# Kernel optimization log

Hardware: AMD Instinct MI355X
Metric: run time of the kernel (lower is better)

The kernel has to match this reference:

```python
import jax, jax.numpy as jnp
import numpy as np

N_NODES = 100000
N_EDGES = 1600000
D_IN, D_HID, D_LAT = 128, 128, 64


def setup_inputs() -> dict:
    key = jax.random.key(0)
    ks = jax.random.split(key, 8)
    x = jax.random.normal(ks[0], (N_NODES, D_IN), dtype=jnp.float32)
    edge_index = jax.random.randint(ks[1], (2, N_EDGES), 0, N_NODES, dtype=jnp.int64)
    s1 = 1.0 / np.sqrt(D_IN)
    s2 = 1.0 / np.sqrt(D_HID)
    return {
        "x": x,
        "edge_index": edge_index,
        "W1_l": jax.random.normal(ks[2], (D_IN, D_HID), dtype=jnp.float32) * s1,
        "W1_r": jax.random.normal(ks[3], (D_IN, D_HID), dtype=jnp.float32) * s1,
        "b1": jnp.zeros((D_HID,), dtype=jnp.float32),
        "W2_l": jax.random.normal(ks[4], (D_HID, D_LAT), dtype=jnp.float32) * s2,
        "W2_r": jax.random.normal(ks[5], (D_HID, D_LAT), dtype=jnp.float32) * s2,
        "b2": jnp.zeros((D_LAT,), dtype=jnp.float32),
    }


def _sage_conv_mean(x, src, dst, W_l, W_r, b):
    """PyG SAGEConv with mean aggregation: lin_l(mean_j x_j) + lin_r(x_i)."""
    n = x.shape[0]
    # scatter-mean of source features into destination nodes
    agg = jax.ops.segment_sum(x[src], dst, num_segments=n)           # [N, d]
    deg = jax.ops.segment_sum(jnp.ones_like(dst, dtype=x.dtype), dst, num_segments=n)
    mean = agg / jnp.maximum(deg, 1.0)[:, None]
    return mean @ W_l + b + x @ W_r


def reference(x, edge_index, W1_l, W1_r, b1, W2_l, W2_r, b2):
    src, dst = edge_index[0], edge_index[1]
    h = jax.nn.relu(_sage_conv_mean(x, src, dst, W1_l, W1_r, b1))
    # Dropout(p=0.2) is identity in eval mode
    z = jax.nn.relu(_sage_conv_mean(h, src, dst, W2_l, W2_r, b2))
    return z
```

## Files before the change

kernel.cpp:

```cpp
#include <hip/hip_runtime.h>

#define N_NODES 100000
#define N_EDGES 1600000
#define D_IN 128
#define D_HID 128
#define D_LAT 64

#define BSHIFT 8
#define NB 392
#define CAP 4608
#define EPB 4096
#define PART_BLOCKS ((N_EDGES + EPB - 1) / EPB)

typedef unsigned short ushort_t;
typedef unsigned int uint_t;
typedef unsigned char uchar_t;
using bf16x8 = __attribute__((ext_vector_type(8))) short;
using f32x4  = __attribute__((ext_vector_type(4))) float;
using f32x2  = __attribute__((ext_vector_type(2))) float;

__device__ inline ushort_t f2bf(float f) {
    uint_t u = __float_as_uint(f);
    return (ushort_t)((u + 0x7fffu + ((u >> 16) & 1u)) >> 16);
}
__device__ inline uint_t pack2bf(float a, float b) {
    return (uint_t)f2bf(a) | ((uint_t)f2bf(b) << 16);
}
__device__ inline float bf2f(ushort_t u) {
    return __uint_as_float(((uint_t)u) << 16);
}

#if __has_builtin(__builtin_amdgcn_cvt_pk_f32_fp8) && __has_builtin(__builtin_amdgcn_cvt_pk_fp8_f32)
#define HW_FP8 1
template<bool HI>
__device__ inline f32x2 fp8pk2f(uint_t v) {
    return __builtin_amdgcn_cvt_pk_f32_fp8(v, HI);
}
__device__ inline uint_t f2fp8pk4(float a, float b, float c, float d) {
    uint_t w = __builtin_amdgcn_cvt_pk_fp8_f32(a, b, 0, false);
    w = __builtin_amdgcn_cvt_pk_fp8_f32(c, d, w, true);
    return w;
}
__device__ inline uchar_t f2fp8_byte(float f) {
    return (uchar_t)(__builtin_amdgcn_cvt_pk_fp8_f32(f, f, 0, false) & 0xff);
}
#else
__device__ inline float fp8b2f(uint_t b) {
    uint_t em = b & 0x7f;
    if (em == 0) return 0.f;
    uint_t bits = ((em << 20) + (120u << 23)) | ((b & 0x80u) << 24);
    return __uint_as_float(bits);
}
template<bool HI>
__device__ inline f32x2 fp8pk2f(uint_t v) {
    uint_t w = HI ? (v >> 16) : v;
    f32x2 r; r.x = fp8b2f(w & 0xff); r.y = fp8b2f((w >> 8) & 0xff);
    return r;
}
__device__ inline uint_t f2fp8_1(float f) {
    uint_t u = __float_as_uint(f);
    uint_t s = (u >> 31) << 7;
    uint_t au = u & 0x7fffffff;
    if (au >= 0x43e00000u) return s | 0x7e;
    if (au < 0x3c000000u) return s;
    uint_t r = au + 0x0007ffffu + ((au >> 20) & 1u);
    return s | (((r >> 20) - (120u << 3)) & 0x7f);
}
__device__ inline uint_t f2fp8pk4(float a, float b, float c, float d) {
    return f2fp8_1(a) | (f2fp8_1(b) << 8) | (f2fp8_1(c) << 16) | (f2fp8_1(d) << 24);
}
__device__ inline uchar_t f2fp8_byte(float f) { return (uchar_t)f2fp8_1(f); }
#endif

__device__ inline void accf8x4(float* a, uint_t w, int base) {
    f32x2 p0 = fp8pk2f<false>(w);
    f32x2 p1 = fp8pk2f<true>(w);
    a[base + 0] += p0.x; a[base + 1] += p0.y;
    a[base + 2] += p1.x; a[base + 3] += p1.y;
}
__device__ inline void accf8x16(float* a, uint4 u) {
    accf8x4(a, u.x, 0); accf8x4(a, u.y, 4); accf8x4(a, u.z, 8); accf8x4(a, u.w, 12);
}

__device__ inline void pack_w256(const float* Wl, const float* Wr, ushort_t* pack,
                                 int N, int tid) {
    int lane = tid & 63;
    int t = tid >> 6;
    int kt = t & 7;
    int nt = t >> 3;
    int n = nt * 16 + (lane & 15);
    int kbase = kt * 32 + (lane >> 4) * 8;
    ushort_t v[8];
    #pragma unroll
    for (int j = 0; j < 8; ++j) {
        int k = kbase + j;
        float w = (k < 128) ? Wl[k * N + n] : Wr[(k - 128) * N + n];
        v[j] = f2bf(w);
    }
    *(uint4*)(pack + (long)tid * 8) = *(uint4*)v;
}
__device__ inline void pack_w128(const float* W, ushort_t* pack, int N, int tid) {
    int lane = tid & 63;
    int t = tid >> 6;
    int kt = t & 3;
    int nt = t >> 2;
    int n = nt * 16 + (lane & 15);
    int kbase = kt * 32 + (lane >> 4) * 8;
    ushort_t v[8];
    #pragma unroll
    for (int j = 0; j < 8; ++j) v[j] = f2bf(W[(kbase + j) * N + n]);
    *(uint4*)(pack + (long)tid * 8) = *(uint4*)v;
}

__global__ __launch_bounds__(256) void prep_kernel(
        const float* __restrict__ W1_l, const float* __restrict__ W1_r,
        ushort_t* __restrict__ pack1,
        const float* __restrict__ W2_l, ushort_t* __restrict__ pack2l,
        const float* __restrict__ W2_r, ushort_t* __restrict__ pack2r,
        int* __restrict__ gCur) {
    int b = blockIdx.x;
    if (b < 16) {
        pack_w256(W1_l, W1_r, pack1, 128, b * 256 + threadIdx.x);
    } else if (b < 20) {
        pack_w128(W2_l, pack2l, 64, (b - 16) * 256 + threadIdx.x);
    } else if (b < 24) {
        pack_w128(W2_r, pack2r, 64, (b - 20) * 256 + threadIdx.x);
    } else {
        int t = (b - 24) * 256 + threadIdx.x;
        if (t < NB) gCur[t] = t * CAP;
    }
}

__global__ __launch_bounds__(256) void bucket_scatter_kernel(const int* __restrict__ src,
                                                             const int* __restrict__ dst,
                                                             int* __restrict__ gCur,
                                                             int* __restrict__ bedges) {
    __shared__ int h[NB];
    __shared__ int start[NB];
    for (int j = threadIdx.x; j < NB; j += 256) h[j] = 0;
    __syncthreads();
    long base = (long)blockIdx.x * EPB + threadIdx.x * 16;
    int dc[16], sc[16];
    int cnt = 0;
    if (base + 16 <= N_EDGES) {
        #pragma unroll
        for (int j = 0; j < 4; ++j) {
            int4 d4 = *(const int4*)(dst + base + j * 4);
            int4 s4 = *(const int4*)(src + base + j * 4);
            dc[j * 4 + 0] = d4.x; dc[j * 4 + 1] = d4.y; dc[j * 4 + 2] = d4.z; dc[j * 4 + 3] = d4.w;
            sc[j * 4 + 0] = s4.x; sc[j * 4 + 1] = s4.y; sc[j * 4 + 2] = s4.z; sc[j * 4 + 3] = s4.w;
        }
        cnt = 16;
    } else if (base < N_EDGES) {
        cnt = (int)(N_EDGES - base);
        for (int j = 0; j < cnt; ++j) { dc[j] = dst[base + j]; sc[j] = src[base + j]; }
    }
    for (int j = 0; j < cnt; ++j) atomicAdd(&h[dc[j] >> BSHIFT], 1);
    __syncthreads();
    for (int j = threadIdx.x; j < NB; j += 256)
        start[j] = h[j] ? atomicAdd(&gCur[j], h[j]) : 0;
    __syncthreads();
    for (int j = 0; j < cnt; ++j) {
        int b = dc[j] >> BSHIFT;
        int p = atomicAdd(&start[b], 1);
        if (p < (b + 1) * CAP)
            bedges[p] = ((dc[j] & 255) << 24) | sc[j];
    }
}

__global__ __launch_bounds__(256) void bucket_sort_kernel(const int* __restrict__ gCur,
                                                          const int* __restrict__ bedges,
                                                          int* __restrict__ csr,
                                                          int2* __restrict__ off2) {
    __shared__ int sdata[256];
    __shared__ int cur[256];
    int b = blockIdx.x, t = threadIdx.x;
    int r0 = b * CAP;
    int n = gCur[b] - r0;
    if (n > CAP) n = CAP;
    cur[t] = 0;
    __syncthreads();
    for (int k = t * 4; k < n; k += 1024) {
        int4 v4 = *(const int4*)(bedges + r0 + k);
        int m = n - k;
        atomicAdd(&cur[(unsigned)v4.x >> 24], 1);
        if (m > 1) atomicAdd(&cur[(unsigned)v4.y >> 24], 1);
        if (m > 2) atomicAdd(&cur[(unsigned)v4.z >> 24], 1);
        if (m > 3) atomicAdd(&cur[(unsigned)v4.w >> 24], 1);
    }
    __syncthreads();
    int c = cur[t];
    sdata[t] = c;
    __syncthreads();
    for (int d = 1; d < 256; d <<= 1) {
        int u = (t >= d) ? sdata[t - d] : 0;
        __syncthreads();
        sdata[t] += u;
        __syncthreads();
    }
    int ex = (t == 0) ? 0 : sdata[t - 1];
    off2[(b << BSHIFT) + t] = make_int2(r0 + ex, c);
    cur[t] = ex;
    __syncthreads();
    for (int k = t * 4; k < n; k += 1024) {
        int4 v4 = *(const int4*)(bedges + r0 + k);
        int m = n - k;
        {
            int p = atomicAdd(&cur[(unsigned)v4.x >> 24], 1);
            csr[r0 + p] = v4.x & 0xFFFFFF;
        }
        if (m > 1) {
            int p = atomicAdd(&cur[(unsigned)v4.y >> 24], 1);
            csr[r0 + p] = v4.y & 0xFFFFFF;
        }
        if (m > 2) {
            int p = atomicAdd(&cur[(unsigned)v4.z >> 24], 1);
            csr[r0 + p] = v4.z & 0xFFFFFF;
        }
        if (m > 3) {
            int p = atomicAdd(&cur[(unsigned)v4.w >> 24], 1);
            csr[r0 + p] = v4.w & 0xFFFFFF;
        }
    }
}

__global__ void cvt_both_kernel(const float* __restrict__ in, ushort_t* __restrict__ outb,
                                uchar_t* __restrict__ out8, long n) {
    long i = ((long)blockIdx.x * blockDim.x + threadIdx.x) * 16;
    if (i >= n) return;
    float4 a = *(const float4*)(in + i);
    float4 b = *(const float4*)(in + i + 4);
    float4 c = *(const float4*)(in + i + 8);
    float4 d = *(const float4*)(in + i + 12);
    uint4 ob0, ob1;
    ob0.x = pack2bf(a.x, a.y); ob0.y = pack2bf(a.z, a.w);
    ob0.z = pack2bf(b.x, b.y); ob0.w = pack2bf(b.z, b.w);
    ob1.x = pack2bf(c.x, c.y); ob1.y = pack2bf(c.z, c.w);
    ob1.z = pack2bf(d.x, d.y); ob1.w = pack2bf(d.z, d.w);
    *(uint4*)(outb + i) = ob0;
    *(uint4*)(outb + i + 8) = ob1;
    uint4 o8;
    o8.x = f2fp8pk4(a.x, a.y, a.z, a.w);
    o8.y = f2fp8pk4(b.x, b.y, b.z, b.w);
    o8.z = f2fp8pk4(c.x, c.y, c.z, c.w);
    o8.w = f2fp8pk4(d.x, d.y, d.z, d.w);
    *(uint4*)(out8 + i) = o8;
}

__global__ __launch_bounds__(256) void gather_mean_fp8_kernel(
        const int2* __restrict__ off2, const int* __restrict__ csr_src,
        const uchar_t* __restrict__ x8, ushort_t* __restrict__ mean_out) {
    int lane  = threadIdx.x & 7;
    int local = threadIdx.x >> 3;
    long i = (long)blockIdx.x * 32 + local;
    if (i >= N_NODES) return;
    int2 bd = off2[i];
    int beg = bd.x, n = bd.y;
    const uchar_t* base = x8 + lane * 16;
    float acc[16];
    #pragma unroll
    for (int j = 0; j < 16; ++j) acc[j] = 0.f;
    int k = 0;
    for (; k + 4 <= n; k += 4) {
        int s0 = csr_src[beg + k];
        int s1 = csr_src[beg + k + 1];
        int s2 = csr_src[beg + k + 2];
        int s3 = csr_src[beg + k + 3];
        uint4 u0 = *(const uint4*)(base + (long)s0 * 128);
        uint4 u1 = *(const uint4*)(base + (long)s1 * 128);
        uint4 u2 = *(const uint4*)(base + (long)s2 * 128);
        uint4 u3 = *(const uint4*)(base + (long)s3 * 128);
        accf8x16(acc, u0); accf8x16(acc, u1); accf8x16(acc, u2); accf8x16(acc, u3);
    }
    for (; k < n; ++k) {
        int s0 = csr_src[beg + k];
        uint4 u0 = *(const uint4*)(base + (long)s0 * 128);
        accf8x16(acc, u0);
    }
    float inv = (n > 0) ? 1.f / (float)n : 0.f;
    uint4 o0, o1;
    o0.x = pack2bf(acc[0] * inv,  acc[1] * inv);
    o0.y = pack2bf(acc[2] * inv,  acc[3] * inv);
    o0.z = pack2bf(acc[4] * inv,  acc[5] * inv);
    o0.w = pack2bf(acc[6] * inv,  acc[7] * inv);
    o1.x = pack2bf(acc[8] * inv,  acc[9] * inv);
    o1.y = pack2bf(acc[10] * inv, acc[11] * inv);
    o1.z = pack2bf(acc[12] * inv, acc[13] * inv);
    o1.w = pack2bf(acc[14] * inv, acc[15] * inv);
    ushort_t* mp = mean_out + i * 128 + lane * 16;
    *(uint4*)mp = o0;
    *(uint4*)(mp + 8) = o1;
}

__global__ __launch_bounds__(256) void gather_mean64_fp8_kernel(
        const int2* __restrict__ off2, const int* __restrict__ csr_src,
        const uchar_t* __restrict__ g8, ushort_t* __restrict__ mean_out) {
    int lane  = threadIdx.x & 3;
    int local = threadIdx.x >> 2;
    long i = (long)blockIdx.x * 64 + local;
    if (i >= N_NODES) return;
    int2 bd = off2[i];
    int beg = bd.x, n = bd.y;
    const uchar_t* base = g8 + lane * 16;
    float acc[16];
    #pragma unroll
    for (int j = 0; j < 16; ++j) acc[j] = 0.f;
    int k = 0;
    for (; k + 4 <= n; k += 4) {
        int s0 = csr_src[beg + k];
        int s1 = csr_src[beg + k + 1];
        int s2 = csr_src[beg + k + 2];
        int s3 = csr_src[beg + k + 3];
        uint4 u0 = *(const uint4*)(base + (long)s0 * 64);
        uint4 u1 = *(const uint4*)(base + (long)s1 * 64);
        uint4 u2 = *(const uint4*)(base + (long)s2 * 64);
        uint4 u3 = *(const uint4*)(base + (long)s3 * 64);
        accf8x16(acc, u0); accf8x16(acc, u1); accf8x16(acc, u2); accf8x16(acc, u3);
    }
    for (; k < n; ++k) {
        int s0 = csr_src[beg + k];
        uint4 u0 = *(const uint4*)(base + (long)s0 * 64);
        accf8x16(acc, u0);
    }
    float inv = (n > 0) ? 1.f / (float)n : 0.f;
    uint4 o0, o1;
    o0.x = pack2bf(acc[0] * inv,  acc[1] * inv);
    o0.y = pack2bf(acc[2] * inv,  acc[3] * inv);
    o0.z = pack2bf(acc[4] * inv,  acc[5] * inv);
    o0.w = pack2bf(acc[6] * inv,  acc[7] * inv);
    o1.x = pack2bf(acc[8] * inv,  acc[9] * inv);
    o1.y = pack2bf(acc[10] * inv, acc[11] * inv);
    o1.z = pack2bf(acc[12] * inv, acc[13] * inv);
    o1.w = pack2bf(acc[14] * inv, acc[15] * inv);
    ushort_t* mp = mean_out + i * 64 + lane * 16;
    *(uint4*)mp = o0;
    *(uint4*)(mp + 8) = o1;
}

template<int NOUT, bool OUT_BF16>
__global__ __launch_bounds__(256) void mfma_mlp_kernel(
        const ushort_t* __restrict__ Am, const ushort_t* __restrict__ Ax,
        const ushort_t* __restrict__ pack, const float* __restrict__ bias,
        void* __restrict__ outv) {
    constexpr int NT = NOUT / 16;
    int lane = threadIdx.x & 63;
    int wave = threadIdx.x >> 6;
    long m0 = (long)blockIdx.x * 64 + wave * 16;
    int r = lane & 15;
    int quad = lane >> 4;
    long arow = m0 + r;
    if (arow > N_NODES - 1) arow = N_NODES - 1;

    bf16x8 areg[8];
    #pragma unroll
    for (int kt = 0; kt < 8; ++kt) {
        const ushort_t* s = (kt < 4) ? Am : Ax;
        int k = (kt & 3) * 32 + quad * 8;
        areg[kt] = *(const bf16x8*)(s + arow * 128 + k);
    }

    f32x4 acc[NT];
    #pragma unroll
    for (int nt = 0; nt < NT; ++nt) acc[nt] = (f32x4){0.f, 0.f, 0.f, 0.f};

    #pragma unroll
    for (int nt = 0; nt < NT; ++nt) {
        #pragma unroll
        for (int kt = 0; kt < 8; ++kt) {
            bf16x8 bfrag = *(const bf16x8*)(pack + ((long)(nt * 8 + kt) * 64 + lane) * 8);
            acc[nt] = __builtin_amdgcn_mfma_f32_16x16x32_bf16(areg[kt], bfrag, acc[nt], 0, 0, 0);
        }
    }

    #pragma unroll
    for (int nt = 0; nt < NT; ++nt) {
        int col = nt * 16 + r;
        float bj = bias[col];
        #pragma unroll
        for (int q = 0; q < 4; ++q) {
            long orow = m0 + quad * 4 + q;
            if (orow < N_NODES) {
                float v = fmaxf(acc[nt][q] + bj, 0.f);
                if (OUT_BF16) ((ushort_t*)outv)[orow * NOUT + col] = f2bf(v);
                else          ((float*)outv)[orow * NOUT + col] = v;
            }
        }
    }
}

template<int NOUT, int OUTMODE, bool PRELOAD, bool HASBIAS, bool RELU>
__global__ __launch_bounds__(256) void mfma_gemm_k128_kernel(
        const ushort_t* __restrict__ A, const ushort_t* __restrict__ pack,
        const float* __restrict__ bias, const ushort_t* __restrict__ Cpre,
        void* __restrict__ outv) {
    constexpr int NT = NOUT / 16;
    int lane = threadIdx.x & 63;
    int wave = threadIdx.x >> 6;
    long m0 = (long)blockIdx.x * 64 + wave * 16;
    int r = lane & 15;
    int quad = lane >> 4;
    long arow = m0 + r;
    if (arow > N_NODES - 1) arow = N_NODES - 1;

    bf16x8 areg[4];
    #pragma unroll
    for (int kt = 0; kt < 4; ++kt)
        areg[kt] = *(const bf16x8*)(A + arow * 128 + kt * 32 + quad * 8);

    f32x4 acc[NT];
    #pragma unroll
    for (int nt = 0; nt < NT; ++nt) {
        if (PRELOAD) {
            int col = nt * 16 + r;
            #pragma unroll
            for (int q = 0; q < 4; ++q) {
                long row = m0 + quad * 4 + q;
                if (row > N_NODES - 1) row = N_NODES - 1;
                acc[nt][q] = bf2f(Cpre[row * NOUT + col]);
            }
        } else {
            acc[nt] = (f32x4){0.f, 0.f, 0.f, 0.f};
        }
    }

    #pragma unroll
    for (int nt = 0; nt < NT; ++nt) {
        #pragma unroll
        for (int kt = 0; kt < 4; ++kt) {
            bf16x8 bfrag = *(const bf16x8*)(pack + ((long)(nt * 4 + kt) * 64 + lane) * 8);
            acc[nt] = __builtin_amdgcn_mfma_f32_16x16x32_bf16(areg[kt], bfrag, acc[nt], 0, 0, 0);
        }
    }

    #pragma unroll
    for (int nt = 0; nt < NT; ++nt) {
        int col = nt * 16 + r;
        float bj = HASBIAS ? bias[col] : 0.f;
        #pragma unroll
        for (int q = 0; q < 4; ++q) {
            long orow = m0 + quad * 4 + q;
            if (orow < N_NODES) {
                float v = acc[nt][q] + bj;
                if (RELU) v = fmaxf(v, 0.f);
                if (OUTMODE == 2)      ((uchar_t*)outv)[orow * NOUT + col] = f2fp8_byte(v);
                else if (OUTMODE == 1) ((ushort_t*)outv)[orow * NOUT + col] = f2bf(v);
                else                   ((float*)outv)[orow * NOUT + col] = v;
            }
        }
    }
}

extern "C" void kernel_launch(void* const* d_in, const int* in_sizes, int n_in,
                              void* d_out, int out_size, void* d_ws, size_t ws_size,
                              hipStream_t stream) {
    const float* x    = (const float*)d_in[0];
    const int*   ei   = (const int*)d_in[1];
    const float* W1_l = (const float*)d_in[2];
    const float* W1_r = (const float*)d_in[3];
    const float* b1   = (const float*)d_in[4];
    const float* W2_l = (const float*)d_in[5];
    const float* W2_r = (const float*)d_in[6];
    const float* b2   = (const float*)d_in[7];
    float* out = (float*)d_out;

    const int* src = ei;
    const int* dst = ei + N_EDGES;

    int*  gCur   = (int*)d_ws;
    int2* off2   = (int2*)(gCur + 512);
    int*  bedges = (int*)(off2 + 100608);
    int*  csr    = bedges + NB * CAP;
    ushort_t* xb    = (ushort_t*)(csr + NB * CAP);
    ushort_t* mean1 = xb + (long)N_NODES * 128;
    uchar_t*  g8    = (uchar_t*)mean1;
    ushort_t* meang = mean1 + (long)N_NODES * 64;
    ushort_t* hb    = mean1 + (long)N_NODES * 128;
    uchar_t*  x8    = (uchar_t*)hb;
    ushort_t* pack1  = hb + (long)N_NODES * 128;
    ushort_t* pack2l = pack1 + 256 * 128;
    ushort_t* pack2r = pack2l + 128 * 64;

    prep_kernel<<<26, 256, 0, stream>>>(W1_l, W1_r, pack1, W2_l, pack2l, W2_r, pack2r, gCur);

    bucket_scatter_kernel<<<PART_BLOCKS, 256, 0, stream>>>(src, dst, gCur, bedges);
    bucket_sort_kernel<<<NB, 256, 0, stream>>>(gCur, bedges, csr, off2);

    cvt_both_kernel<<<((long)N_NODES * 128 / 16 + 255) / 256, 256, 0, stream>>>(
        x, xb, x8, (long)N_NODES * 128);

    gather_mean_fp8_kernel<<<(N_NODES + 31) / 32, 256, 0, stream>>>(off2, csr, x8, mean1);
    mfma_mlp_kernel<128, true><<<(N_NODES + 63) / 64, 256, 0, stream>>>(mean1, xb, pack1, b1, hb);

    mfma_gemm_k128_kernel<64, 2, false, false, false><<<(N_NODES + 63) / 64, 256, 0, stream>>>(
        hb, pack2l, nullptr, nullptr, g8);
    gather_mean64_fp8_kernel<<<(N_NODES + 63) / 64, 256, 0, stream>>>(off2, csr, g8, meang);
    mfma_gemm_k128_kernel<64, 0, true, true, true><<<(N_NODES + 63) / 64, 256, 0, stream>>>(
        hb, pack2r, b2, meang, out);
}
```

Baseline: 262.6 us.

## Fuse conversion into prep, layer-1 MLP with W2_l GEMM, and gather with final GEMM

Folds the x-to-bf16/fp8 conversion into the weight-prep launch. The layer-1 MLP kernel now stages its h tile in shared memory and immediately applies W2_l to produce the fp8 g tensor, so hb is not re-read for that GEMM. The second-layer gather-mean is merged with the final W2_r GEMM through a shared-memory mean tile, which removes the meang round trip through global memory and cuts two launches. In exchange the fused kernels use more shared memory and registers, which may lower occupancy, and the final kernel couples an irregular gather with MFMA work.

New measurement: 246.1 us (median of 2 runs). 1.07x faster.

```diff
diff --git a/kernel.cpp b/kernel.cpp
--- a/kernel.cpp
+++ b/kernel.cpp
@@ -11,6 +11,7 @@
 #define CAP 4608
 #define EPB 4096
 #define PART_BLOCKS ((N_EDGES + EPB - 1) / EPB)
+#define CVT_BLOCKS (((long)N_NODES * 128 / 16 + 255) / 256)
 
 typedef unsigned short ushort_t;
 typedef unsigned int uint_t;
@@ -117,7 +118,9 @@
         ushort_t* __restrict__ pack1,
         const float* __restrict__ W2_l, ushort_t* __restrict__ pack2l,
         const float* __restrict__ W2_r, ushort_t* __restrict__ pack2r,
-        int* __restrict__ gCur) {
+        int* __restrict__ gCur,
+        const float* __restrict__ x, ushort_t* __restrict__ xb,
+        uchar_t* __restrict__ x8) {
     int b = blockIdx.x;
     if (b < 16) {
         pack_w256(W1_l, W1_r, pack1, 128, b * 256 + threadIdx.x);
@@ -125,9 +128,29 @@
         pack_w128(W2_l, pack2l, 64, (b - 16) * 256 + threadIdx.x);
     } else if (b < 24) {
         pack_w128(W2_r, pack2r, 64, (b - 20) * 256 + threadIdx.x);
-    } else {
+    } else if (b < 26) {
         int t = (b - 24) * 256 + threadIdx.x;
         if (t < NB) gCur[t] = t * CAP;
+    } else {
+        long i = ((long)(b - 26) * 256 + threadIdx.x) * 16;
+        if (i >= (long)N_NODES * 128) return;
+        float4 a = *(const float4*)(x + i);
+        float4 bb = *(const float4*)(x + i + 4);
+        float4 c = *(const float4*)(x + i + 8);
+        float4 d = *(const float4*)(x + i + 12);
+        uint4 ob0, ob1;
+        ob0.x = pack2bf(a.x, a.y);  ob0.y = pack2bf(a.z, a.w);
+        ob0.z = pack2bf(bb.x, bb.y); ob0.w = pack2bf(bb.z, bb.w);
+        ob1.x = pack2bf(c.x, c.y);  ob1.y = pack2bf(c.z, c.w);
+        ob1.z = pack2bf(d.x, d.y);  ob1.w = pack2bf(d.z, d.w);
+        *(uint4*)(xb + i) = ob0;
+        *(uint4*)(xb + i + 8) = ob1;
+        uint4 o8;
+        o8.x = f2fp8pk4(a.x, a.y, a.z, a.w);
+        o8.y = f2fp8pk4(bb.x, bb.y, bb.z, bb.w);
+        o8.z = f2fp8pk4(c.x, c.y, c.z, c.w);
+        o8.w = f2fp8pk4(d.x, d.y, d.z, d.w);
+        *(uint4*)(x8 + i) = o8;
     }
 }
 
@@ -222,29 +245,6 @@
             csr[r0 + p] = v4.w & 0xFFFFFF;
         }
     }
-}
-
-__global__ void cvt_both_kernel(const float* __restrict__ in, ushort_t* __restrict__ outb,
-                                uchar_t* __restrict__ out8, long n) {
-    long i = ((long)blockIdx.x * blockDim.x + threadIdx.x) * 16;
-    if (i >= n) return;
-    float4 a = *(const float4*)(in + i);
-    float4 b = *(const float4*)(in + i + 4);
-    float4 c = *(const float4*)(in + i + 8);
-    float4 d = *(const float4*)(in + i + 12);
-    uint4 ob0, ob1;
-    ob0.x = pack2bf(a.x, a.y); ob0.y = pack2bf(a.z, a.w);
-    ob0.z = pack2bf(b.x, b.y); ob0.w = pack2bf(b.z, b.w);
-    ob1.x = pack2bf(c.x, c.y); ob1.y = pack2bf(c.z, c.w);
-    ob1.z = pack2bf(d.x, d.y); ob1.w = pack2bf(d.z, d.w);
-    *(uint4*)(outb + i) = ob0;
-    *(uint4*)(outb + i + 8) = ob1;
-    uint4 o8;
-    o8.x = f2fp8pk4(a.x, a.y, a.z, a.w);
-    o8.y = f2fp8pk4(b.x, b.y, b.z, b.w);
-    o8.z = f2fp8pk4(c.x, c.y, c.z, c.w);
-    o8.w = f2fp8pk4(d.x, d.y, d.z, d.w);
-    *(uint4*)(out8 + i) = o8;
 }
 
 __global__ __launch_bounds__(256) void gather_mean_fp8_kernel(
@@ -292,57 +292,13 @@
     *(uint4*)(mp + 8) = o1;
 }
 
-__global__ __launch_bounds__(256) void gather_mean64_fp8_kernel(
-        const int2* __restrict__ off2, const int* __restrict__ csr_src,
-        const uchar_t* __restrict__ g8, ushort_t* __restrict__ mean_out) {
-    int lane  = threadIdx.x & 3;
-    int local = threadIdx.x >> 2;
-    long i = (long)blockIdx.x * 64 + local;
-    if (i >= N_NODES) return;
-    int2 bd = off2[i];
-    int beg = bd.x, n = bd.y;
-    const uchar_t* base = g8 + lane * 16;
-    float acc[16];
-    #pragma unroll
-    for (int j = 0; j < 16; ++j) acc[j] = 0.f;
-    int k = 0;
-    for (; k + 4 <= n; k += 4) {
-        int s0 = csr_src[beg + k];
-        int s1 = csr_src[beg + k + 1];
-        int s2 = csr_src[beg + k + 2];
-        int s3 = csr_src[beg + k + 3];
-        uint4 u0 = *(const uint4*)(base + (long)s0 * 64);
-        uint4 u1 = *(const uint4*)(base + (long)s1 * 64);
-        uint4 u2 = *(const uint4*)(base + (long)s2 * 64);
-        uint4 u3 = *(const uint4*)(base + (long)s3 * 64);
-        accf8x16(acc, u0); accf8x16(acc, u1); accf8x16(acc, u2); accf8x16(acc, u3);
-    }
-    for (; k < n; ++k) {
-        int s0 = csr_src[beg + k];
-        uint4 u0 = *(const uint4*)(base + (long)s0 * 64);
-        accf8x16(acc, u0);
-    }
-    float inv = (n > 0) ? 1.f / (float)n : 0.f;
-    uint4 o0, o1;
-    o0.x = pack2bf(acc[0] * inv,  acc[1] * inv);
-    o0.y = pack2bf(acc[2] * inv,  acc[3] * inv);
-    o0.z = pack2bf(acc[4] * inv,  acc[5] * inv);
-    o0.w = pack2bf(acc[6] * inv,  acc[7] * inv);
-    o1.x = pack2bf(acc[8] * inv,  acc[9] * inv);
-    o1.y = pack2bf(acc[10] * inv, acc[11] * inv);
-    o1.z = pack2bf(acc[12] * inv, acc[13] * inv);
-    o1.w = pack2bf(acc[14] * inv, acc[15] * inv);
-    ushort_t* mp = mean_out + i * 64 + lane * 16;
-    *(uint4*)mp = o0;
-    *(uint4*)(mp + 8) = o1;
-}
-
-template<int NOUT, bool OUT_BF16>
-__global__ __launch_bounds__(256) void mfma_mlp_kernel(
+#define HSTRIDE 132
+__global__ __launch_bounds__(256) void mfma_mlp_fused_kernel(
         const ushort_t* __restrict__ Am, const ushort_t* __restrict__ Ax,
-        const ushort_t* __restrict__ pack, const float* __restrict__ bias,
-        void* __restrict__ outv) {
-    constexpr int NT = NOUT / 16;
+        const ushort_t* __restrict__ pack1, const float* __restrict__ bias,
+        const ushort_t* __restrict__ pack2l,
+        ushort_t* __restrict__ hb, uchar_t* __restrict__ g8) {
+    __shared__ ushort_t htile[4][16 * HSTRIDE];
     int lane = threadIdx.x & 63;
     int wave = threadIdx.x >> 6;
     long m0 = (long)blockIdx.x * 64 + wave * 16;
@@ -359,93 +315,148 @@
         areg[kt] = *(const bf16x8*)(s + arow * 128 + k);
     }
 
-    f32x4 acc[NT];
-    #pragma unroll
-    for (int nt = 0; nt < NT; ++nt) acc[nt] = (f32x4){0.f, 0.f, 0.f, 0.f};
-
-    #pragma unroll
-    for (int nt = 0; nt < NT; ++nt) {
+    f32x4 acc[8];
+    #pragma unroll
+    for (int nt = 0; nt < 8; ++nt) acc[nt] = (f32x4){0.f, 0.f, 0.f, 0.f};
+    #pragma unroll
+    for (int nt = 0; nt < 8; ++nt) {
         #pragma unroll
         for (int kt = 0; kt < 8; ++kt) {
-            bf16x8 bfrag = *(const bf16x8*)(pack + ((long)(nt * 8 + kt) * 64 + lane) * 8);
+            bf16x8 bfrag = *(const bf16x8*)(pack1 + ((long)(nt * 8 + kt) * 64 + lane) * 8);
             acc[nt] = __builtin_amdgcn_mfma_f32_16x16x32_bf16(areg[kt], bfrag, acc[nt], 0, 0, 0);
         }
     }
 
     #pragma unroll
-    for (int nt = 0; nt < NT; ++nt) {
+    for (int nt = 0; nt < 8; ++nt) {
         int col = nt * 16 + r;
         float bj = bias[col];
         #pragma unroll
         for (int q = 0; q < 4; ++q) {
             long orow = m0 + quad * 4 + q;
-            if (orow < N_NODES) {
-                float v = fmaxf(acc[nt][q] + bj, 0.f);
-                if (OUT_BF16) ((ushort_t*)outv)[orow * NOUT + col] = f2bf(v);
-                else          ((float*)outv)[orow * NOUT + col] = v;
-            }
-        }
-    }
-}
-
-template<int NOUT, int OUTMODE, bool PRELOAD, bool HASBIAS, bool RELU>
-__global__ __launch_bounds__(256) void mfma_gemm_k128_kernel(
-        const ushort_t* __restrict__ A, const ushort_t* __restrict__ pack,
-        const float* __restrict__ bias, const ushort_t* __restrict__ Cpre,
-        void* __restrict__ outv) {
-    constexpr int NT = NOUT / 16;
+            float v = fmaxf(acc[nt][q] + bj, 0.f);
+            ushort_t hv = f2bf(v);
+            if (orow < N_NODES) hb[orow * 128 + col] = hv;
+            htile[wave][(quad * 4 + q) * HSTRIDE + col] = hv;
+        }
+    }
+    bf16x8 areg2[4];
+    #pragma unroll
+    for (int kt = 0; kt < 4; ++kt)
+        areg2[kt] = *(const bf16x8*)(&htile[wave][r * HSTRIDE + kt * 32 + quad * 8]);
+    f32x4 gacc[4];
+    #pragma unroll
+    for (int nt = 0; nt < 4; ++nt) gacc[nt] = (f32x4){0.f, 0.f, 0.f, 0.f};
+    #pragma unroll
+    for (int nt = 0; nt < 4; ++nt) {
+        #pragma unroll
+        for (int kt = 0; kt < 4; ++kt) {
+            bf16x8 bfrag = *(const bf16x8*)(pack2l + ((long)(nt * 4 + kt) * 64 + lane) * 8);
+            gacc[nt] = __builtin_amdgcn_mfma_f32_16x16x32_bf16(areg2[kt], bfrag, gacc[nt], 0, 0, 0);
+        }
+    }
+    #pragma unroll
+    for (int nt = 0; nt < 4; ++nt) {
+        int col = nt * 16 + r;
+        #pragma unroll
+        for (int q = 0; q < 4; ++q) {
+            long orow = m0 + quad * 4 + q;
+            if (orow < N_NODES) g8[orow * 64 + col] = f2fp8_byte(gacc[nt][q]);
+        }
+    }
+}
+
+#define MSTRIDE 68
+__global__ __launch_bounds__(256) void mfma_final_kernel(
+        const int2* __restrict__ off2, const int* __restrict__ csr_src,
+        const uchar_t* __restrict__ g8,
+        const ushort_t* __restrict__ hb, const ushort_t* __restrict__ pack2r,
+        const float* __restrict__ b2, float* __restrict__ out) {
+    __shared__ ushort_t mtile[64 * MSTRIDE];
+    long m0 = (long)blockIdx.x * 64;
+    {
+        int lane  = threadIdx.x & 3;
+        int local = threadIdx.x >> 2;
+        long i = m0 + local;
+        if (i > N_NODES - 1) i = N_NODES - 1;
+        int2 bd = off2[i];
+        int beg = bd.x, n = bd.y;
+        const uchar_t* base = g8 + lane * 16;
+        float acc[16];
+        #pragma unroll
+        for (int j = 0; j < 16; ++j) acc[j] = 0.f;
+        int k = 0;
+        for (; k + 4 <= n; k += 4) {
+            int s0 = csr_src[beg + k];
+            int s1 = csr_src[beg + k + 1];
+            int s2 = csr_src[beg + k + 2];
+            int s3 = csr_src[beg + k + 3];
+            uint4 u0 = *(const uint4*)(base + (long)s0 * 64);
+            uint4 u1 = *(const uint4*)(base + (long)s1 * 64);
+            uint4 u2 = *(const uint4*)(base + (long)s2 * 64);
+            uint4 u3 = *(const uint4*)(base + (long)s3 * 64);
+            accf8x16(acc, u0); accf8x16(acc, u1); accf8x16(acc, u2); accf8x16(acc, u3);
+        }
+        for (; k < n; ++k) {
+            int s0 = csr_src[beg + k];
+            uint4 u0 = *(const uint4*)(base + (long)s0 * 64);
+            accf8x16(acc, u0);
+        }
+        float inv = (n > 0) ? 1.f / (float)n : 0.f;
+        uint4 o0, o1;
+        o0.x = pack2bf(acc[0] * inv,  acc[1] * inv);
+        o0.y = pack2bf(acc[2] * inv,  acc[3] * inv);
+        o0.z = pack2bf(acc[4] * inv,  acc[5] * inv);
+        o0.w = pack2bf(acc[6] * inv,  acc[7] * inv);
+        o1.x = pack2bf(acc[8] * inv,  acc[9] * inv);
+        o1.y = pack2bf(acc[10] * inv, acc[11] * inv);
+        o1.z = pack2bf(acc[12] * inv, acc[13] * inv);
+        o1.w = pack2bf(acc[14] * inv, acc[15] * inv);
+        ushort_t* mp = mtile + local * MSTRIDE + lane * 16;
+        *(uint4*)mp = o0;
+        *(uint4*)(mp + 8) = o1;
+    }
+    __syncthreads();
     int lane = threadIdx.x & 63;
     int wave = threadIdx.x >> 6;
-    long m0 = (long)blockIdx.x * 64 + wave * 16;
+    long mw = m0 + wave * 16;
     int r = lane & 15;
     int quad = lane >> 4;
-    long arow = m0 + r;
+    long arow = mw + r;
     if (arow > N_NODES - 1) arow = N_NODES - 1;
 
     bf16x8 areg[4];
     #pragma unroll
     for (int kt = 0; kt < 4; ++kt)
-        areg[kt] = *(const bf16x8*)(A + arow * 128 + kt * 32 + quad * 8);
-
-    f32x4 acc[NT];
-    #pragma unroll
-    for (int nt = 0; nt < NT; ++nt) {
-        if (PRELOAD) {
-            int col = nt * 16 + r;
-            #pragma unroll
-            for (int q = 0; q < 4; ++q) {
-                long row = m0 + quad * 4 + q;
-                if (row > N_NODES - 1) row = N_NODES - 1;
-                acc[nt][q] = bf2f(Cpre[row * NOUT + col]);
-            }
-        } else {
-            acc[nt] = (f32x4){0.f, 0.f, 0.f, 0.f};
-        }
-    }
-
-    #pragma unroll
-    for (int nt = 0; nt < NT; ++nt) {
+        areg[kt] = *(const bf16x8*)(hb + arow * 128 + kt * 32 + quad * 8);
+
+    f32x4 acc[4];
+    #pragma unroll
+    for (int nt = 0; nt < 4; ++nt) {
+        int col = nt * 16 + r;
+        #pragma unroll
+        for (int q = 0; q < 4; ++q) {
+            int rowl = wave * 16 + quad * 4 + q;
+            acc[nt][q] = bf2f(mtile[rowl * MSTRIDE + col]);
+        }
+    }
+    #pragma unroll
+    for (int nt = 0; nt < 4; ++nt) {
         #pragma unroll
         for (int kt = 0; kt < 4; ++kt) {
-            bf16x8 bfrag = *(const bf16x8*)(pack + ((long)(nt * 4 + kt) * 64 + lane) * 8);
+            bf16x8 bfrag = *(const bf16x8*)(pack2r + ((long)(nt * 4 + kt) * 64 + lane) * 8);
             acc[nt] = __builtin_amdgcn_mfma_f32_16x16x32_bf16(areg[kt], bfrag, acc[nt], 0, 0, 0);
         }
     }
-
-    #pragma unroll
-    for (int nt = 0; nt < NT; ++nt) {
+    #pragma unroll
+    for (int nt = 0; nt < 4; ++nt) {
         int col = nt * 16 + r;
-        float bj = HASBIAS ? bias[col] : 0.f;
+        float bj = b2[col];
         #pragma unroll
         for (int q = 0; q < 4; ++q) {
-            long orow = m0 + quad * 4 + q;
-            if (orow < N_NODES) {
-                float v = acc[nt][q] + bj;
-                if (RELU) v = fmaxf(v, 0.f);
-                if (OUTMODE == 2)      ((uchar_t*)outv)[orow * NOUT + col] = f2fp8_byte(v);
-                else if (OUTMODE == 1) ((ushort_t*)outv)[orow * NOUT + col] = f2bf(v);
-                else                   ((float*)outv)[orow * NOUT + col] = v;
-            }
+            long orow = mw + quad * 4 + q;
+            if (orow < N_NODES)
+                out[orow * 64 + col] = fmaxf(acc[nt][q] + bj, 0.f);
         }
     }
 }
@@ -472,28 +483,23 @@
     int*  csr    = bedges + NB * CAP;
     ushort_t* xb    = (ushort_t*)(csr + NB * CAP);
     ushort_t* mean1 = xb + (long)N_NODES * 128;
-    uchar_t*  g8    = (uchar_t*)mean1;
-    ushort_t* meang = mean1 + (long)N_NODES * 64;
     ushort_t* hb    = mean1 + (long)N_NODES * 128;
     uchar_t*  x8    = (uchar_t*)hb;
     ushort_t* pack1  = hb + (long)N_NODES * 128;
     ushort_t* pack2l = pack1 + 256 * 128;
     ushort_t* pack2r = pack2l + 128 * 64;
-
-    prep_kernel<<<26, 256, 0, stream>>>(W1_l, W1_r, pack1, W2_l, pack2l, W2_r, pack2r, gCur);
+    uchar_t*  g8     = (uchar_t*)(pack2r + 128 * 64);
+
+    prep_kernel<<<26 + CVT_BLOCKS, 256, 0, stream>>>(
+        W1_l, W1_r, pack1, W2_l, pack2l, W2_r, pack2r, gCur, x, xb, x8);
 
     bucket_scatter_kernel<<<PART_BLOCKS, 256, 0, stream>>>(src, dst, gCur, bedges);
     bucket_sort_kernel<<<NB, 256, 0, stream>>>(gCur, bedges, csr, off2);
 
-    cvt_both_kernel<<<((long)N_NODES * 128 / 16 + 255) / 256, 256, 0, stream>>>(
-        x, xb, x8, (long)N_NODES * 128);
-
     gather_mean_fp8_kernel<<<(N_NODES + 31) / 32, 256, 0, stream>>>(off2, csr, x8, mean1);
-    mfma_mlp_kernel<128, true><<<(N_NODES + 63) / 64, 256, 0, stream>>>(mean1, xb, pack1, b1, hb);
-
-    mfma_gemm_k128_kernel<64, 2, false, false, false><<<(N_NODES + 63) / 64, 256, 0, stream>>>(
-        hb, pack2l, nullptr, nullptr, g8);
-    gather_mean64_fp8_kernel<<<(N_NODES + 63) / 64, 256, 0, stream>>>(off2, csr, g8, meang);
-    mfma_gemm_k128_kernel<64, 0, true, true, true><<<(N_NODES + 63) / 64, 256, 0, stream>>>(
-        hb, pack2r, b2, meang, out);
-}
+    mfma_mlp_fused_kernel<<<(N_NODES + 63) / 64, 256, 0, stream>>>(
+        mean1, xb, pack1, b1, pack2l, hb, g8);
+
+    mfma_final_kernel<<<(N_NODES + 63) / 64, 256, 0, stream>>>(
+        off2, csr, g8, hb, pack2r, b2, out);
+}
```
